# Performance work log

Hardware: AMD Instinct MI355X
Metric: run time of the kernel (lower is better)

Reference implementation:

```python
import jax, jax.numpy as jnp
import numpy as np

N, E, D = 50000, 800000, 128
H, C = 8, 16  # heads, hidden_per_head; H*C == D
NEG_SLOPE = 0.15


def setup_inputs() -> dict:
    key = jax.random.key(0)
    ks = jax.random.split(key, 8)
    x = jax.random.normal(ks[0], (N, D), dtype=jnp.float32)
    edge_index = jax.random.randint(ks[1], (2, E), 0, N, dtype=jnp.int32)
    s = 1.0 / np.sqrt(D)
    return {
        "x": x,
        "edge_index": edge_index,
        "ln_g": jnp.ones((D,), jnp.float32),
        "ln_b": jnp.zeros((D,), jnp.float32),
        "W_l": jax.random.normal(ks[2], (D, H * C), jnp.float32) * s,
        "b_l": jnp.zeros((H * C,), jnp.float32),
        "W_r": jax.random.normal(ks[3], (D, H * C), jnp.float32) * s,
        "b_r": jnp.zeros((H * C,), jnp.float32),
        "att": jax.random.normal(ks[4], (H, C), jnp.float32) * (1.0 / np.sqrt(C)),
        "bias": jnp.zeros((H * C,), jnp.float32),
    }


def _layernorm(x, g, b, eps=1e-5):
    mu = jnp.mean(x, axis=-1, keepdims=True)
    var = jnp.mean(jnp.square(x - mu), axis=-1, keepdims=True)
    return (x - mu) * jax.lax.rsqrt(var + eps) * g + b


def reference(x, edge_index, ln_g, ln_b, W_l, b_l, W_r, b_r, att, bias):
    src, dst = edge_index[0], edge_index[1]
    h = _layernorm(x, ln_g, ln_b)                      # [N, D]
    xl = (h @ W_l + b_l).reshape(N, H, C)              # source-side transform
    xr = (h @ W_r + b_r).reshape(N, H, C)              # target-side transform
    # GATv2 edge attention: leaky_relu(x_j + x_i) . att
    e = xl[src] + xr[dst]                              # [E, H, C]
    e_act = jnp.where(e > 0, e, NEG_SLOPE * e)
    alpha = jnp.einsum('ehc,hc->eh', e_act, att)       # [E, H]
    # segment softmax over edges grouped by destination node
    m = jax.ops.segment_max(alpha, dst, num_segments=N)   # [N, H]
    ex = jnp.exp(alpha - m[dst])                           # [E, H]
    denom = jax.ops.segment_sum(ex, dst, num_segments=N)  # [N, H]
    a = ex / (denom[dst] + 1e-16)                          # [E, H]
    # weighted message aggregation (scatter-add)
    msg = xl[src] * a[:, :, None]                          # [E, H, C]
    out = jax.ops.segment_sum(msg, dst, num_segments=N)   # [N, H, C]
    out = out.reshape(N, H * C) + bias
    h2 = jax.nn.relu(out)                                  # act='relu', dropout off (eval)
    return x + h2                                          # proj is Identity (in_dim == out_dim)
```

## Files before the change

### kernel.cpp

```cpp
#include <hip/hip_runtime.h>

typedef unsigned int uint32;
typedef __attribute__((ext_vector_type(4))) float f32x4;
typedef __attribute__((ext_vector_type(2))) float f32x2;
typedef __attribute__((ext_vector_type(8))) short bf16x8;

#define NEG_SLOPE 0.15f
#define GPB 1

__device__ __forceinline__ float2 bf2_to_f2(uint32 u) {
  union { uint32 i; float f; } a, b;
  a.i = u << 16;
  b.i = u & 0xffff0000u;
  return make_float2(a.f, b.f);
}

__device__ __forceinline__ f32x2 unpk(uint32 u) {
  union { uint32 i; float f; } lo, hi;
  lo.i = u << 16; hi.i = u & 0xffff0000u;
  f32x2 r; r.x = lo.f; r.y = hi.f; return r;
}

__device__ __forceinline__ f32x2 vmax2(f32x2 a, f32x2 b) {
  f32x2 r; r.x = fmaxf(a.x, b.x); r.y = fmaxf(a.y, b.y); return r;
}

__device__ __forceinline__ float bf_to_f(unsigned short s) {
  union { uint32 i; float f; } u;
  u.i = ((uint32)s) << 16;
  return u.f;
}

__device__ __forceinline__ unsigned short f32_to_bf16(float f) {
  union { float f; uint32 i; } u; u.f = f;
  uint32 r = u.i + 0x7fffu + ((u.i >> 16) & 1u);
  return (unsigned short)(r >> 16);
}

__device__ __forceinline__ uint32 pack_bf2(float x, float y) {
  return (uint32)f32_to_bf16(x) | ((uint32)f32_to_bf16(y) << 16);
}

__device__ __forceinline__ float2 loadpair(const void* p, size_t i, int isbf) {
  if (isbf) return bf2_to_f2(((const uint32*)p)[i]);
  return ((const float2*)p)[i];
}

__device__ __forceinline__ float loadelem(const void* p, size_t i, int isbf) {
  if (isbf) return bf_to_f(((const unsigned short*)p)[i]);
  return ((const float*)p)[i];
}

__device__ __forceinline__ int get_isbf(const void* ln_g) {
  return ((const uint32*)ln_g)[0] != 0x3F800000u ? 1 : 0;
}

__global__ __launch_bounds__(256) void prepAll_k(
    const void* __restrict__ Wl, const void* __restrict__ Wr,
    const void* __restrict__ bl, const void* __restrict__ br,
    const void* __restrict__ att, const void* __restrict__ obias,
    const void* __restrict__ ln_g, const void* __restrict__ ln_b,
    unsigned short* __restrict__ Wt, float* __restrict__ c1,
    float* __restrict__ c2b, float* __restrict__ att_c,
    float* __restrict__ obias_c)
{
  int isbf = get_isbf(ln_g);
  int b = blockIdx.x;
  if (b < 128) {
    int id = b * 256 + threadIdx.x;
    int n = id >> 7, k = id & 127;
    float g = loadelem(ln_g, k, isbf);
    float v = (n < 128) ? loadelem(Wl, (size_t)k * 128 + n, isbf)
                        : loadelem(Wr, (size_t)k * 128 + (n - 128), isbf);
    Wt[(size_t)n * 128 + k] = f32_to_bf16(g * v);
    if (id < 128) {
      att_c[id]   = loadelem(att, id, isbf);
      obias_c[id] = loadelem(obias, id, isbf);
    }
  } else {
    int w = threadIdx.x >> 6, lane = threadIdx.x & 63;
    int n = (b - 128) * 4 + w;
    const void* W = (n < 128) ? Wl : Wr;
    int nn = n & 127;
    float s1 = 0.f, s2 = 0.f;
    #pragma unroll
    for (int t = 0; t < 2; ++t) {
      int kk = t * 64 + lane;
      float wv = loadelem(W, (size_t)kk * 128 + nn, isbf);
      s1 += loadelem(ln_g, kk, isbf) * wv;
      s2 += loadelem(ln_b, kk, isbf) * wv;
    }
    #pragma unroll
    for (int off = 1; off < 64; off <<= 1) {
      s1 += __shfl_xor(s1, off, 64);
      s2 += __shfl_xor(s2, off, 64);
    }
    if (lane == 0) {
      c1[n] = s1;
      c2b[n] = s2 + ((n < 128) ? loadelem(bl, nn, isbf) : loadelem(br, nn, isbf));
    }
  }
}

__device__ __forceinline__ void load_group(bf16x8* slot, const void* x,
                                           int isbf, int rl, int quad) {
  if (isbf) {
    const unsigned short* xp = (const unsigned short*)x + (size_t)rl * 128 + quad * 8;
    #pragma unroll
    for (int kc = 0; kc < 4; ++kc) slot[kc] = *(const bf16x8*)(xp + kc * 32);
  } else {
    const float* xp = (const float*)x + (size_t)rl * 128 + quad * 8;
    #pragma unroll
    for (int kc = 0; kc < 4; ++kc) {
      float4 a0 = *(const float4*)(xp + kc * 32);
      float4 a1 = *(const float4*)(xp + kc * 32 + 4);
      union { bf16x8 v; uint32 u[4]; } av;
      av.u[0] = pack_bf2(a0.x, a0.y);
      av.u[1] = pack_bf2(a0.z, a0.w);
      av.u[2] = pack_bf2(a1.x, a1.y);
      av.u[3] = pack_bf2(a1.z, a1.w);
      slot[kc] = av.v;
    }
  }
}

__global__ __launch_bounds__(256) void ln_gemm_k(
    const void* __restrict__ x, const void* __restrict__ ln_g,
    const unsigned short* __restrict__ Wt,
    const float* __restrict__ c1, const float* __restrict__ c2b,
    unsigned short* __restrict__ xl,
    unsigned short* __restrict__ xr,
    int nrows)
{
  int isbf = get_isbf(ln_g);
  int lane = threadIdx.x & 63;
  int w    = threadIdx.x >> 6;
  int m16  = lane & 15;
  int quad = lane >> 4;
  int base = blockIdx.x * (GPB * 16);

  bf16x8 araw[GPB][4];
  #pragma unroll
  for (int g2 = 0; g2 < GPB; ++g2) {
    int r = base + g2 * 16 + m16;
    if (r >= nrows) r = nrows - 1;
    load_group(araw[g2], x, isbf, r, quad);
  }

  bf16x8 bfrag[4][4];
  #pragma unroll
  for (int nt = 0; nt < 4; ++nt)
    #pragma unroll
    for (int kc = 0; kc < 4; ++kc)
      bfrag[nt][kc] = *(const bf16x8*)(
          Wt + (size_t)(w * 64 + nt * 16 + m16) * 128 + kc * 32 + quad * 8);

  float c1v[4], c2v[4];
  #pragma unroll
  for (int nt = 0; nt < 4; ++nt) {
    int col = w * 64 + nt * 16 + m16;
    c1v[nt] = c1[col];
    c2v[nt] = c2b[col];
  }

  unsigned short* dst = (w < 2) ? xl : xr;
  int cb = (w & 1) * 64;

  #pragma unroll
  for (int g2 = 0; g2 < GPB; ++g2) {
    bf16x8* A = araw[g2];

    float s = 0.f, s2 = 0.f;
    #pragma unroll
    for (int kc = 0; kc < 4; ++kc) {
      union { bf16x8 v; uint32 u[4]; } uu; uu.v = A[kc];
      #pragma unroll
      for (int j = 0; j < 4; ++j) {
        float2 t = bf2_to_f2(uu.u[j]);
        s += t.x + t.y;
        s2 += t.x * t.x + t.y * t.y;
      }
    }
    s  += __shfl_xor(s, 16, 64);  s2 += __shfl_xor(s2, 16, 64);
    s  += __shfl_xor(s, 32, 64);  s2 += __shfl_xor(s2, 32, 64);
    float mu  = s * (1.0f / 128.0f);
    float var = fmaxf(s2 * (1.0f / 128.0f) - mu * mu, 0.0f);
    float rs  = rsqrtf(var + 1e-5f);
    float rm  = rs * mu;

    f32x4 acc[4];
    #pragma unroll
    for (int nt = 0; nt < 4; ++nt) acc[nt] = (f32x4){0.f, 0.f, 0.f, 0.f};
    #pragma unroll
    for (int kc = 0; kc < 4; ++kc)
      #pragma unroll
      for (int nt = 0; nt < 4; ++nt)
        acc[nt] = __builtin_amdgcn_mfma_f32_16x16x32_bf16(A[kc], bfrag[nt][kc], acc[nt], 0, 0, 0);

    float rs_j[4], rm_j[4];
    #pragma unroll
    for (int j = 0; j < 4; ++j) {
      rs_j[j] = __shfl(rs, quad * 4 + j, 64);
      rm_j[j] = __shfl(rm, quad * 4 + j, 64);
    }

    #pragma unroll
    for (int nt = 0; nt < 4; ++nt) {
      #pragma unroll
      for (int j = 0; j < 4; ++j) {
        int r = base + g2 * 16 + quad * 4 + j;
        if (r < nrows)
          dst[(size_t)r * 128 + cb + nt * 16 + m16] =
              f32_to_bf16(rs_j[j] * acc[nt][j] - rm_j[j] * c1v[nt] + c2v[nt]);
      }
    }
  }
}

__global__ __launch_bounds__(256) void hist_k(
    const int* __restrict__ ei, int* __restrict__ cntg,
    int E, int Eb, int R)
{
  __shared__ int hist[256];
  int b = blockIdx.x, tid = threadIdx.x;
  hist[tid] = 0;
  __syncthreads();
  int startE = b * Eb, endE = min(E, startE + Eb);
  const int* dp = ei + E;
  if (((E | startE) & 3) == 0) {
    int nfull = (endE - startE) >> 2;
    for (int g = tid; g < nfull; g += 256) {
      int4 d = *(const int4*)(dp + startE + g * 4);
      atomicAdd(&hist[((uint32)d.x) >> 8], 1);
      atomicAdd(&hist[((uint32)d.y) >> 8], 1);
      atomicAdd(&hist[((uint32)d.z) >> 8], 1);
      atomicAdd(&hist[((uint32)d.w) >> 8], 1);
    }
    int rem0 = startE + nfull * 4;
    if (rem0 + tid < endE) atomicAdd(&hist[((uint32)dp[rem0 + tid]) >> 8], 1);
  } else {
    for (int e = startE + tid; e < endE; e += 256)
      atomicAdd(&hist[((uint32)dp[e]) >> 8], 1);
  }
  __syncthreads();
  if (tid < R) cntg[tid * 256 + b] = hist[tid];
}

__global__ __launch_bounds__(1024) void scanA_k(const int* __restrict__ in,
    int* __restrict__ outl, int* __restrict__ psum, int n)
{
  __shared__ int wsum[16];
  int tid = threadIdx.x, lane = tid & 63, w = tid >> 6;
  int i = blockIdx.x * 1024 + tid;
  int v = (i < n) ? in[i] : 0;
  int xs = v;
  #pragma unroll
  for (int off = 1; off < 64; off <<= 1) {
    int y = __shfl_up(xs, off, 64);
    if (lane >= off) xs += y;
  }
  if (lane == 63) wsum[w] = xs;
  __syncthreads();
  if (w == 0) {
    int sv = (lane < 16) ? wsum[lane] : 0;
    int ss = sv;
    #pragma unroll
    for (int off = 1; off < 16; off <<= 1) {
      int y = __shfl_up(ss, off, 64);
      if (lane >= off) ss += y;
    }
    if (lane < 16) wsum[lane] = ss - sv;
    if (lane == 15) psum[blockIdx.x] = ss;
  }
  __syncthreads();
  if (i < n) outl[i] = wsum[w] + xs - v;
}

__global__ void scanB_k(int* __restrict__ psum, int* __restrict__ total, int nb) {
  int lane = threadIdx.x;
  int v = (lane < nb) ? psum[lane] : 0;
  int xs = v;
  #pragma unroll
  for (int off = 1; off < 64; off <<= 1) {
    int y = __shfl_up(xs, off, 64);
    if (lane >= off) xs += y;
  }
  if (lane < nb) psum[lane] = xs - v;
  if (lane == 63) *total = xs;
}

__global__ void scanC2_k(int* __restrict__ arr, const int* __restrict__ psum, int n) {
  int i = blockIdx.x * blockDim.x + threadIdx.x;
  if (i < n) arr[i] += psum[i >> 10];
}

__global__ __launch_bounds__(256) void binscatter_k(
    const int* __restrict__ ei, const int* __restrict__ cbase,
    uint32* __restrict__ binned, int E, int Eb, int R)
{
  __shared__ int cur[256];
  int b = blockIdx.x, tid = threadIdx.x;
  if (tid < R) cur[tid] = cbase[tid * 256 + b];
  __syncthreads();
  int startE = b * Eb, endE = min(E, startE + Eb);
  if (((E | startE) & 3) == 0) {
    int nfull = (endE - startE) >> 2;
    for (int g = tid; g < nfull; g += 256) {
      int e = startE + g * 4;
      int4 s = *(const int4*)(ei + e);
      int4 d = *(const int4*)(ei + E + e);
      int p0 = atomicAdd(&cur[((uint32)d.x) >> 8], 1);
      binned[p0] = (uint32)s.x | (((uint32)d.x & 255u) << 16);
      int p1 = atomicAdd(&cur[((uint32)d.y) >> 8], 1);
      binned[p1] = (uint32)s.y | (((uint32)d.y & 255u) << 16);
      int p2 = atomicAdd(&cur[((uint32)d.z) >> 8], 1);
      binned[p2] = (uint32)s.z | (((uint32)d.z & 255u) << 16);
      int p3 = atomicAdd(&cur[((uint32)d.w) >> 8], 1);
      binned[p3] = (uint32)s.w | (((uint32)d.w & 255u) << 16);
    }
    int rem0 = startE + nfull * 4;
    if (rem0 + tid < endE) {
      int e = rem0 + tid;
      uint32 src = (uint32)ei[e], dst = (uint32)ei[E + e];
      int pos = atomicAdd(&cur[dst >> 8], 1);
      binned[pos] = src | ((dst & 255u) << 16);
    }
  } else {
    for (int e = startE + tid; e < endE; e += 256) {
      uint32 src = (uint32)ei[e], dst = (uint32)ei[E + e];
      int pos = atomicAdd(&cur[dst >> 8], 1);
      binned[pos] = src | ((dst & 255u) << 16);
    }
  }
}

__global__ __launch_bounds__(256) void rangesort_k(
    const uint32* __restrict__ binned, const int* __restrict__ cbase,
    int* __restrict__ starts, unsigned short* __restrict__ csr16,
    int E, int N, int R)
{
  __shared__ int hist[256];
  __shared__ int wsum[4];
  __shared__ int cur[256];
  int r = blockIdx.x;
  int tid = threadIdx.x, lane = tid & 63, w = tid >> 6;
  int segStart = cbase[r * 256];
  int segEnd = (r + 1 < R) ? cbase[(r + 1) * 256] : E;

  hist[tid] = 0;
  __syncthreads();
  for (int i = segStart + tid; i < segEnd; i += 256)
    atomicAdd(&hist[(binned[i] >> 16) & 255u], 1);
  __syncthreads();

  int v = hist[tid];
  int xs = v;
  #pragma unroll
  for (int off = 1; off < 64; off <<= 1) {
    int y = __shfl_up(xs, off, 64);
    if (lane >= off) xs += y;
  }
  if (lane == 63) wsum[w] = xs;
  __syncthreads();
  int woff = 0;
  #pragma unroll
  for (int i = 0; i < 4; ++i) if (i < w) woff += wsum[i];
  int st = segStart + woff + xs - v;
  int node = (r << 8) + tid;
  if (node < N) starts[node] = st;
  cur[tid] = st;
  __syncthreads();

  for (int i = segStart + tid; i < segEnd; i += 256) {
    uint32 pk = binned[i];
    int d = (pk >> 16) & 255u;
    int pos = atomicAdd(&cur[d], 1);
    csr16[pos] = (unsigned short)(pk & 0xffffu);
  }
}

__global__ __launch_bounds__(256) void agg_k(
    const uint32* __restrict__ xl32,
    const uint32* __restrict__ xr32,
    const int* __restrict__ starts, const unsigned short* __restrict__ csr16,
    const void* __restrict__ x, const void* __restrict__ ln_g,
    const float* __restrict__ att_c, const float* __restrict__ obias_c,
    void* __restrict__ out, int n)
{
  int node = blockIdx.x * 4 + (threadIdx.x >> 6);
  if (node >= n) return;
  int isbf = get_isbf(ln_g);
  int lane = threadIdx.x & 63;
  int q    = lane >> 4;
  int sub  = lane & 15;

  uint4 xru = *(const uint4*)(xr32 + (size_t)node * 64 + sub * 4);
  f32x2 xr0 = unpk(xru.x), xr1 = unpk(xru.y), xr2 = unpk(xru.z), xr3 = unpk(xru.w);
  const f32x2* atp = (const f32x2*)(att_c + sub * 8);
  f32x2 t0 = atp[0], t1 = atp[1], t2 = atp[2], t3 = atp[3];
  f32x2 ns; ns.x = NEG_SLOPE; ns.y = NEG_SLOPE;

  float lsum = 0.f;
  f32x2 ac[4];
  #pragma unroll
  for (int i = 0; i < 4; ++i) { ac[i].x = 0.f; ac[i].y = 0.f; }

  int p0 = starts[node], p1 = starts[node + 1];
  if (p0 < p1) {
    int pmax = p1 - 1;
    int pe = p0 + q;
    bool valid = pe < p1;
    uint4 xu = *(const uint4*)(xl32 + (size_t)csr16[min(pe, pmax)] * 64 + sub * 4);

    for (int p = p0; p < p1; p += 4) {
      int pen = p + 4 + q;
      uint4 xun = *(const uint4*)(xl32 + (size_t)csr16[min(pen, pmax)] * 64 + sub * 4);

      f32x2 a0 = unpk(xu.x), a1 = unpk(xu.y), a2 = unpk(xu.z), a3 = unpk(xu.w);
      f32x2 e0 = a0 + xr0, e1 = a1 + xr1, e2 = a2 + xr2, e3 = a3 + xr3;
      e0 = vmax2(e0, e0 * ns);
      e1 = vmax2(e1, e1 * ns);
      e2 = vmax2(e2, e2 * ns);
      e3 = vmax2(e3, e3 * ns);
      f32x2 dt = e0 * t0;
      dt += e1 * t1;
      dt += e2 * t2;
      dt += e3 * t3;
      float dot = dt.x + dt.y;
      dot += __shfl_xor(dot, 1, 64);
      float pw = valid ? __expf(dot) : 0.f;
      lsum += pw;
      f32x2 pw2; pw2.x = pw; pw2.y = pw;
      ac[0] += pw2 * a0;
      ac[1] += pw2 * a1;
      ac[2] += pw2 * a2;
      ac[3] += pw2 * a3;

      xu = xun;
      valid = pen < p1;
    }
  }

  lsum += __shfl_xor(lsum, 16, 64);
  lsum += __shfl_xor(lsum, 32, 64);
  #pragma unroll
  for (int i = 0; i < 4; ++i) {
    ac[i].x += __shfl_xor(ac[i].x, 16, 64);
    ac[i].x += __shfl_xor(ac[i].x, 32, 64);
    ac[i].y += __shfl_xor(ac[i].y, 16, 64);
    ac[i].y += __shfl_xor(ac[i].y, 32, 64);
  }

  if (q == 0) {
    float inv = 1.0f / (lsum + 1e-16f);
    float4 b0 = *(const float4*)(obias_c + sub * 8);
    float4 b1 = *(const float4*)(obias_c + sub * 8 + 4);
    float2 rx[4];
    #pragma unroll
    for (int i = 0; i < 4; ++i)
      rx[i] = loadpair(x, (size_t)node * 64 + sub * 4 + i, isbf);
    float o0 = rx[0].x + fmaxf(ac[0].x * inv + b0.x, 0.f);
    float o1 = rx[0].y + fmaxf(ac[0].y * inv + b0.y, 0.f);
    float o2 = rx[1].x + fmaxf(ac[1].x * inv + b0.z, 0.f);
    float o3 = rx[1].y + fmaxf(ac[1].y * inv + b0.w, 0.f);
    float o4 = rx[2].x + fmaxf(ac[2].x * inv + b1.x, 0.f);
    float o5 = rx[2].y + fmaxf(ac[2].y * inv + b1.y, 0.f);
    float o6 = rx[3].x + fmaxf(ac[3].x * inv + b1.z, 0.f);
    float o7 = rx[3].y + fmaxf(ac[3].y * inv + b1.w, 0.f);
    if (isbf) {
      uint4 ov;
      ov.x = pack_bf2(o0, o1); ov.y = pack_bf2(o2, o3);
      ov.z = pack_bf2(o4, o5); ov.w = pack_bf2(o6, o7);
      *(uint4*)((uint32*)out + (size_t)node * 64 + sub * 4) = ov;
    } else {
      float4 f0 = make_float4(o0, o1, o2, o3);
      float4 f1 = make_float4(o4, o5, o6, o7);
      *(float4*)((float*)out + (size_t)node * 128 + sub * 8) = f0;
      *(float4*)((float*)out + (size_t)node * 128 + sub * 8 + 4) = f1;
    }
  }
}

static inline char* align16(char* p) {
  return (char*)(((uintptr_t)p + 15) & ~(uintptr_t)15);
}

extern "C" void kernel_launch(void* const* d_in, const int* in_sizes, int n_in,
                              void* d_out, int out_size, void* d_ws, size_t ws_size,
                              hipStream_t stream) {
  const void* x    = d_in[0];
  const int*  ei   = (const int*)d_in[1];
  const void* ln_g = d_in[2];
  const void* ln_b = d_in[3];
  const void* Wl   = d_in[4];
  const void* bl   = d_in[5];
  const void* Wr   = d_in[6];
  const void* br   = d_in[7];
  const void* att  = d_in[8];
  const void* bias = d_in[9];

  int N = in_sizes[0] / 128;
  int E = in_sizes[1] / 2;
  int R = (N + 255) >> 8;
  int L = R * 256;
  int Eb = (((E + 255) / 256) + 3) & ~3;

  char* ws = (char*)d_ws;
  unsigned short* xl = (unsigned short*)ws; ws = align16(ws + (size_t)N * 128 * 2);
  unsigned short* xr = (unsigned short*)ws; ws = align16(ws + (size_t)N * 128 * 2);
  unsigned short* Wt = (unsigned short*)ws; ws = align16(ws + 256 * 128 * 2);
  float* c1      = (float*)ws;              ws = align16(ws + 256 * 4);
  float* c2b     = (float*)ws;              ws = align16(ws + 256 * 4);
  float* att_c   = (float*)ws;              ws = align16(ws + 128 * 4);
  float* obias_c = (float*)ws;              ws = align16(ws + 128 * 4);
  int* cntg      = (int*)ws;                ws = align16(ws + (size_t)L * 4);
  int* cbase     = (int*)ws;                ws = align16(ws + (size_t)L * 4);
  int* psum      = (int*)ws;                ws = align16(ws + 64 * 4);
  int* starts    = (int*)ws;                ws = align16(ws + (size_t)(N + 1) * 4);
  uint32* binned = (uint32*)ws;             ws = align16(ws + (size_t)E * 4);
  unsigned short* csr16 = (unsigned short*)ws; ws = align16(ws + (size_t)E * 2);

  int nbScan = (L + 1023) / 1024;

  hipLaunchKernelGGL(prepAll_k, dim3(192), dim3(256), 0, stream,
                     Wl, Wr, bl, br, att, bias, ln_g, ln_b,
                     Wt, c1, c2b, att_c, obias_c);
  hipLaunchKernelGGL(hist_k, dim3(256), dim3(256), 0, stream, ei, cntg, E, Eb, R);
  hipLaunchKernelGGL(scanA_k, dim3(nbScan), dim3(1024), 0, stream, cntg, cbase, psum, L);
  hipLaunchKernelGGL(scanB_k, dim3(1), dim3(64), 0, stream, psum, starts + N, nbScan);
  hipLaunchKernelGGL(scanC2_k, dim3((L + 255) / 256), dim3(256), 0, stream, cbase, psum, L);
  hipLaunchKernelGGL(binscatter_k, dim3(256), dim3(256), 0, stream,
                     ei, cbase, binned, E, Eb, R);
  hipLaunchKernelGGL(rangesort_k, dim3(R), dim3(256), 0, stream,
                     binned, cbase, starts, csr16, E, N, R);
  hipLaunchKernelGGL(ln_gemm_k, dim3((N + GPB * 16 - 1) / (GPB * 16)), dim3(256), 0, stream,
                     x, ln_g, Wt, c1, c2b, xl, xr, N);
  hipLaunchKernelGGL(agg_k, dim3((N + 3) / 4), dim3(256), 0, stream,
                     (const uint32*)xl, (const uint32*)xr, starts, csr16,
                     x, ln_g, att_c, obias_c, d_out, N);
}
```

Measured before the change: 202.2 us.

## Fuse prep with histogram and binscatter with LN-GEMM, deepen agg prefetch

Merges the weight-prep kernel with the edge histogram into one launch, and the bin-scatter kernel with the layernorm+GEMM into one heterogeneous grid. The scan-add pass is removed by folding the block prefix into the consumers (binscatter and rangesort). GEMM blocks now process two row groups each, and the aggregation loop prefetches two edges ahead instead of one. This reduces launch count and serialization gaps and lets independent work overlap, at the cost of more register pressure. It also drops the unaligned fallback paths in the histogram and scatter kernels.

```diff
diff --git a/kernel.cpp b/kernel.cpp
--- a/kernel.cpp
+++ b/kernel.cpp
@@ -6,7 +6,7 @@
 typedef __attribute__((ext_vector_type(8))) short bf16x8;
 
 #define NEG_SLOPE 0.15f
-#define GPB 1
+#define GPB 2
 
 __device__ __forceinline__ float2 bf2_to_f2(uint32 u) {
   union { uint32 i; float f; } a, b;
@@ -55,18 +55,20 @@
   return ((const uint32*)ln_g)[0] != 0x3F800000u ? 1 : 0;
 }
 
-__global__ __launch_bounds__(256) void prepAll_k(
+__global__ __launch_bounds__(256) void prep_hist_k(
     const void* __restrict__ Wl, const void* __restrict__ Wr,
     const void* __restrict__ bl, const void* __restrict__ br,
     const void* __restrict__ att, const void* __restrict__ obias,
     const void* __restrict__ ln_g, const void* __restrict__ ln_b,
     unsigned short* __restrict__ Wt, float* __restrict__ c1,
     float* __restrict__ c2b, float* __restrict__ att_c,
-    float* __restrict__ obias_c)
+    float* __restrict__ obias_c,
+    const int* __restrict__ ei, int* __restrict__ cntg,
+    int E, int Eb, int R)
 {
-  int isbf = get_isbf(ln_g);
   int b = blockIdx.x;
   if (b < 128) {
+    int isbf = get_isbf(ln_g);
     int id = b * 256 + threadIdx.x;
     int n = id >> 7, k = id & 127;
     float g = loadelem(ln_g, k, isbf);
@@ -77,7 +79,8 @@
       att_c[id]   = loadelem(att, id, isbf);
       obias_c[id] = loadelem(obias, id, isbf);
     }
-  } else {
+  } else if (b < 192) {
+    int isbf = get_isbf(ln_g);
     int w = threadIdx.x >> 6, lane = threadIdx.x & 63;
     int n = (b - 128) * 4 + w;
     const void* W = (n < 128) ? Wl : Wr;
@@ -99,7 +102,69 @@
       c1[n] = s1;
       c2b[n] = s2 + ((n < 128) ? loadelem(bl, nn, isbf) : loadelem(br, nn, isbf));
     }
-  }
+  } else {
+    __shared__ int hist[256];
+    int hb = b - 192, tid = threadIdx.x;
+    hist[tid] = 0;
+    __syncthreads();
+    int startE = hb * Eb, endE = min(E, startE + Eb);
+    const int* dp = ei + E;
+    int nfull = (endE > startE) ? ((endE - startE) >> 2) : 0;
+    for (int g = tid; g < nfull; g += 256) {
+      int4 d = *(const int4*)(dp + startE + g * 4);
+      atomicAdd(&hist[((uint32)d.x) >> 8], 1);
+      atomicAdd(&hist[((uint32)d.y) >> 8], 1);
+      atomicAdd(&hist[((uint32)d.z) >> 8], 1);
+      atomicAdd(&hist[((uint32)d.w) >> 8], 1);
+    }
+    int rem0 = startE + nfull * 4;
+    if (rem0 + tid < endE) atomicAdd(&hist[((uint32)dp[rem0 + tid]) >> 8], 1);
+    __syncthreads();
+    if (tid < R) cntg[tid * 256 + hb] = hist[tid];
+  }
+}
+
+__global__ __launch_bounds__(1024) void scanA_k(const int* __restrict__ in,
+    int* __restrict__ outl, int* __restrict__ psum, int n)
+{
+  __shared__ int wsum[16];
+  int tid = threadIdx.x, lane = tid & 63, w = tid >> 6;
+  int i = blockIdx.x * 1024 + tid;
+  int v = (i < n) ? in[i] : 0;
+  int xs = v;
+  #pragma unroll
+  for (int off = 1; off < 64; off <<= 1) {
+    int y = __shfl_up(xs, off, 64);
+    if (lane >= off) xs += y;
+  }
+  if (lane == 63) wsum[w] = xs;
+  __syncthreads();
+  if (w == 0) {
+    int sv = (lane < 16) ? wsum[lane] : 0;
+    int ss = sv;
+    #pragma unroll
+    for (int off = 1; off < 16; off <<= 1) {
+      int y = __shfl_up(ss, off, 64);
+      if (lane >= off) ss += y;
+    }
+    if (lane < 16) wsum[lane] = ss - sv;
+    if (lane == 15) psum[blockIdx.x] = ss;
+  }
+  __syncthreads();
+  if (i < n) outl[i] = wsum[w] + xs - v;
+}
+
+__global__ void scanB_k(int* __restrict__ psum, int* __restrict__ total, int nb) {
+  int lane = threadIdx.x;
+  int v = (lane < nb) ? psum[lane] : 0;
+  int xs = v;
+  #pragma unroll
+  for (int off = 1; off < 64; off <<= 1) {
+    int y = __shfl_up(xs, off, 64);
+    if (lane >= off) xs += y;
+  }
+  if (lane < nb) psum[lane] = xs - v;
+  if (lane == 63) *total = xs;
 }
 
 __device__ __forceinline__ void load_group(bf16x8* slot, const void* x,
@@ -124,187 +189,26 @@
   }
 }
 
-__global__ __launch_bounds__(256) void ln_gemm_k(
+__global__ __launch_bounds__(256) void bin_gemm_k(
+    const int* __restrict__ ei, const int* __restrict__ cbase,
+    const int* __restrict__ psum, uint32* __restrict__ binned,
+    int E, int Eb, int R,
     const void* __restrict__ x, const void* __restrict__ ln_g,
     const unsigned short* __restrict__ Wt,
     const float* __restrict__ c1, const float* __restrict__ c2b,
-    unsigned short* __restrict__ xl,
-    unsigned short* __restrict__ xr,
+    unsigned short* __restrict__ xl, unsigned short* __restrict__ xr,
     int nrows)
 {
-  int isbf = get_isbf(ln_g);
-  int lane = threadIdx.x & 63;
-  int w    = threadIdx.x >> 6;
-  int m16  = lane & 15;
-  int quad = lane >> 4;
-  int base = blockIdx.x * (GPB * 16);
-
-  bf16x8 araw[GPB][4];
-  #pragma unroll
-  for (int g2 = 0; g2 < GPB; ++g2) {
-    int r = base + g2 * 16 + m16;
-    if (r >= nrows) r = nrows - 1;
-    load_group(araw[g2], x, isbf, r, quad);
-  }
-
-  bf16x8 bfrag[4][4];
-  #pragma unroll
-  for (int nt = 0; nt < 4; ++nt)
-    #pragma unroll
-    for (int kc = 0; kc < 4; ++kc)
-      bfrag[nt][kc] = *(const bf16x8*)(
-          Wt + (size_t)(w * 64 + nt * 16 + m16) * 128 + kc * 32 + quad * 8);
-
-  float c1v[4], c2v[4];
-  #pragma unroll
-  for (int nt = 0; nt < 4; ++nt) {
-    int col = w * 64 + nt * 16 + m16;
-    c1v[nt] = c1[col];
-    c2v[nt] = c2b[col];
-  }
-
-  unsigned short* dst = (w < 2) ? xl : xr;
-  int cb = (w & 1) * 64;
-
-  #pragma unroll
-  for (int g2 = 0; g2 < GPB; ++g2) {
-    bf16x8* A = araw[g2];
-
-    float s = 0.f, s2 = 0.f;
-    #pragma unroll
-    for (int kc = 0; kc < 4; ++kc) {
-      union { bf16x8 v; uint32 u[4]; } uu; uu.v = A[kc];
-      #pragma unroll
-      for (int j = 0; j < 4; ++j) {
-        float2 t = bf2_to_f2(uu.u[j]);
-        s += t.x + t.y;
-        s2 += t.x * t.x + t.y * t.y;
-      }
-    }
-    s  += __shfl_xor(s, 16, 64);  s2 += __shfl_xor(s2, 16, 64);
-    s  += __shfl_xor(s, 32, 64);  s2 += __shfl_xor(s2, 32, 64);
-    float mu  = s * (1.0f / 128.0f);
-    float var = fmaxf(s2 * (1.0f / 128.0f) - mu * mu, 0.0f);
-    float rs  = rsqrtf(var + 1e-5f);
-    float rm  = rs * mu;
-
-    f32x4 acc[4];
-    #pragma unroll
-    for (int nt = 0; nt < 4; ++nt) acc[nt] = (f32x4){0.f, 0.f, 0.f, 0.f};
-    #pragma unroll
-    for (int kc = 0; kc < 4; ++kc)
-      #pragma unroll
-      for (int nt = 0; nt < 4; ++nt)
-        acc[nt] = __builtin_amdgcn_mfma_f32_16x16x32_bf16(A[kc], bfrag[nt][kc], acc[nt], 0, 0, 0);
-
-    float rs_j[4], rm_j[4];
-    #pragma unroll
-    for (int j = 0; j < 4; ++j) {
-      rs_j[j] = __shfl(rs, quad * 4 + j, 64);
-      rm_j[j] = __shfl(rm, quad * 4 + j, 64);
-    }
-
-    #pragma unroll
-    for (int nt = 0; nt < 4; ++nt) {
-      #pragma unroll
-      for (int j = 0; j < 4; ++j) {
-        int r = base + g2 * 16 + quad * 4 + j;
-        if (r < nrows)
-          dst[(size_t)r * 128 + cb + nt * 16 + m16] =
-              f32_to_bf16(rs_j[j] * acc[nt][j] - rm_j[j] * c1v[nt] + c2v[nt]);
-      }
-    }
-  }
-}
-
-__global__ __launch_bounds__(256) void hist_k(
-    const int* __restrict__ ei, int* __restrict__ cntg,
-    int E, int Eb, int R)
-{
-  __shared__ int hist[256];
-  int b = blockIdx.x, tid = threadIdx.x;
-  hist[tid] = 0;
-  __syncthreads();
-  int startE = b * Eb, endE = min(E, startE + Eb);
-  const int* dp = ei + E;
-  if (((E | startE) & 3) == 0) {
-    int nfull = (endE - startE) >> 2;
-    for (int g = tid; g < nfull; g += 256) {
-      int4 d = *(const int4*)(dp + startE + g * 4);
-      atomicAdd(&hist[((uint32)d.x) >> 8], 1);
-      atomicAdd(&hist[((uint32)d.y) >> 8], 1);
-      atomicAdd(&hist[((uint32)d.z) >> 8], 1);
-      atomicAdd(&hist[((uint32)d.w) >> 8], 1);
-    }
-    int rem0 = startE + nfull * 4;
-    if (rem0 + tid < endE) atomicAdd(&hist[((uint32)dp[rem0 + tid]) >> 8], 1);
-  } else {
-    for (int e = startE + tid; e < endE; e += 256)
-      atomicAdd(&hist[((uint32)dp[e]) >> 8], 1);
-  }
-  __syncthreads();
-  if (tid < R) cntg[tid * 256 + b] = hist[tid];
-}
-
-__global__ __launch_bounds__(1024) void scanA_k(const int* __restrict__ in,
-    int* __restrict__ outl, int* __restrict__ psum, int n)
-{
-  __shared__ int wsum[16];
-  int tid = threadIdx.x, lane = tid & 63, w = tid >> 6;
-  int i = blockIdx.x * 1024 + tid;
-  int v = (i < n) ? in[i] : 0;
-  int xs = v;
-  #pragma unroll
-  for (int off = 1; off < 64; off <<= 1) {
-    int y = __shfl_up(xs, off, 64);
-    if (lane >= off) xs += y;
-  }
-  if (lane == 63) wsum[w] = xs;
-  __syncthreads();
-  if (w == 0) {
-    int sv = (lane < 16) ? wsum[lane] : 0;
-    int ss = sv;
-    #pragma unroll
-    for (int off = 1; off < 16; off <<= 1) {
-      int y = __shfl_up(ss, off, 64);
-      if (lane >= off) ss += y;
-    }
-    if (lane < 16) wsum[lane] = ss - sv;
-    if (lane == 15) psum[blockIdx.x] = ss;
-  }
-  __syncthreads();
-  if (i < n) outl[i] = wsum[w] + xs - v;
-}
-
-__global__ void scanB_k(int* __restrict__ psum, int* __restrict__ total, int nb) {
-  int lane = threadIdx.x;
-  int v = (lane < nb) ? psum[lane] : 0;
-  int xs = v;
-  #pragma unroll
-  for (int off = 1; off < 64; off <<= 1) {
-    int y = __shfl_up(xs, off, 64);
-    if (lane >= off) xs += y;
-  }
-  if (lane < nb) psum[lane] = xs - v;
-  if (lane == 63) *total = xs;
-}
-
-__global__ void scanC2_k(int* __restrict__ arr, const int* __restrict__ psum, int n) {
-  int i = blockIdx.x * blockDim.x + threadIdx.x;
-  if (i < n) arr[i] += psum[i >> 10];
-}
-
-__global__ __launch_bounds__(256) void binscatter_k(
-    const int* __restrict__ ei, const int* __restrict__ cbase,
-    uint32* __restrict__ binned, int E, int Eb, int R)
-{
-  __shared__ int cur[256];
-  int b = blockIdx.x, tid = threadIdx.x;
-  if (tid < R) cur[tid] = cbase[tid * 256 + b];
-  __syncthreads();
-  int startE = b * Eb, endE = min(E, startE + Eb);
-  if (((E | startE) & 3) == 0) {
-    int nfull = (endE - startE) >> 2;
+  if (blockIdx.x < 256) {
+    __shared__ int cur[256];
+    int b = blockIdx.x, tid = threadIdx.x;
+    if (tid < R) {
+      int idx = tid * 256 + b;
+      cur[tid] = cbase[idx] + psum[idx >> 10];
+    }
+    __syncthreads();
+    int startE = b * Eb, endE = min(E, startE + Eb);
+    int nfull = (endE > startE) ? ((endE - startE) >> 2) : 0;
     for (int g = tid; g < nfull; g += 256) {
       int e = startE + g * 4;
       int4 s = *(const int4*)(ei + e);
@@ -325,17 +229,98 @@
       int pos = atomicAdd(&cur[dst >> 8], 1);
       binned[pos] = src | ((dst & 255u) << 16);
     }
-  } else {
-    for (int e = startE + tid; e < endE; e += 256) {
-      uint32 src = (uint32)ei[e], dst = (uint32)ei[E + e];
-      int pos = atomicAdd(&cur[dst >> 8], 1);
-      binned[pos] = src | ((dst & 255u) << 16);
+    return;
+  }
+
+  int bid  = blockIdx.x - 256;
+  int isbf = get_isbf(ln_g);
+  int lane = threadIdx.x & 63;
+  int w    = threadIdx.x >> 6;
+  int m16  = lane & 15;
+  int quad = lane >> 4;
+  int base = bid * (GPB * 16);
+
+  bf16x8 araw[GPB][4];
+  #pragma unroll
+  for (int g2 = 0; g2 < GPB; ++g2) {
+    int r = base + g2 * 16 + m16;
+    if (r >= nrows) r = nrows - 1;
+    load_group(araw[g2], x, isbf, r, quad);
+  }
+
+  bf16x8 bfrag[4][4];
+  #pragma unroll
+  for (int nt = 0; nt < 4; ++nt)
+    #pragma unroll
+    for (int kc = 0; kc < 4; ++kc)
+      bfrag[nt][kc] = *(const bf16x8*)(
+          Wt + (size_t)(w * 64 + nt * 16 + m16) * 128 + kc * 32 + quad * 8);
+
+  float c1v[4], c2v[4];
+  #pragma unroll
+  for (int nt = 0; nt < 4; ++nt) {
+    int col = w * 64 + nt * 16 + m16;
+    c1v[nt] = c1[col];
+    c2v[nt] = c2b[col];
+  }
+
+  unsigned short* dst = (w < 2) ? xl : xr;
+  int cb = (w & 1) * 64;
+
+  #pragma unroll
+  for (int g2 = 0; g2 < GPB; ++g2) {
+    bf16x8* A = araw[g2];
+
+    float s = 0.f, s2 = 0.f;
+    #pragma unroll
+    for (int kc = 0; kc < 4; ++kc) {
+      union { bf16x8 v; uint32 u[4]; } uu; uu.v = A[kc];
+      #pragma unroll
+      for (int j = 0; j < 4; ++j) {
+        float2 t = bf2_to_f2(uu.u[j]);
+        s += t.x + t.y;
+        s2 += t.x * t.x + t.y * t.y;
+      }
+    }
+    s  += __shfl_xor(s, 16, 64);  s2 += __shfl_xor(s2, 16, 64);
+    s  += __shfl_xor(s, 32, 64);  s2 += __shfl_xor(s2, 32, 64);
+    float mu  = s * (1.0f / 128.0f);
+    float var = fmaxf(s2 * (1.0f / 128.0f) - mu * mu, 0.0f);
+    float rs  = rsqrtf(var + 1e-5f);
+    float rm  = rs * mu;
+
+    f32x4 acc[4];
+    #pragma unroll
+    for (int nt = 0; nt < 4; ++nt) acc[nt] = (f32x4){0.f, 0.f, 0.f, 0.f};
+    #pragma unroll
+    for (int kc = 0; kc < 4; ++kc)
+      #pragma unroll
+      for (int nt = 0; nt < 4; ++nt)
+        acc[nt] = __builtin_amdgcn_mfma_f32_16x16x32_bf16(A[kc], bfrag[nt][kc], acc[nt], 0, 0, 0);
+
+    float rs_j[4], rm_j[4];
+    #pragma unroll
+    for (int j = 0; j < 4; ++j) {
+      rs_j[j] = __shfl(rs, quad * 4 + j, 64);
+      rm_j[j] = __shfl(rm, quad * 4 + j, 64);
+    }
+
+    #pragma unroll
+    for (int nt = 0; nt < 4; ++nt) {
+      #pragma unroll
+      for (int j = 0; j < 4; ++j) {
+        int r = base + g2 * 16 + quad * 4 + j;
+        if (r < nrows)
+          dst[(size_t)r * 128 + cb + nt * 16 + m16] =
+              f32_to_bf16(rs_j[j] * acc[nt][j] - rm_j[j] * c1v[nt] + c2v[nt]);
+      }
     }
   }
 }
 
 __global__ __launch_bounds__(256) void rangesort_k(
     const uint32* __restrict__ binned, const int* __restrict__ cbase,
+    const int* __restrict__ psum,
     int* __restrict__ starts, unsigned short* __restrict__ csr16,
     int E, int N, int R)
 {
@@ -344,8 +329,15 @@
   __shared__ int cur[256];
   int r = blockIdx.x;
   int tid = threadIdx.x, lane = tid & 63, w = tid >> 6;
-  int segStart = cbase[r * 256];
-  int segEnd = (r + 1 < R) ? cbase[(r + 1) * 256] : E;
+  int i0 = r * 256;
+  int segStart = cbase[i0] + psum[i0 >> 10];
+  int segEnd;
+  if (r + 1 < R) {
+    int i1 = (r + 1) * 256;
+    segEnd = cbase[i1] + psum[i1 >> 10];
+  } else {
+    segEnd = E;
+  }
 
   hist[tid] = 0;
   __syncthreads();
@@ -408,13 +400,14 @@
   int p0 = starts[node], p1 = starts[node + 1];
   if (p0 < p1) {
     int pmax = p1 - 1;
-    int pe = p0 + q;
-    bool valid = pe < p1;
-    uint4 xu = *(const uint4*)(xl32 + (size_t)csr16[min(pe, pmax)] * 64 + sub * 4);
+    bool v0 = (p0 + q) < p1;
+    bool v1 = (p0 + 4 + q) < p1;
+    uint4 xu  = *(const uint4*)(xl32 + (size_t)csr16[min(p0 + q, pmax)] * 64 + sub * 4);
+    uint4 xu1 = *(const uint4*)(xl32 + (size_t)csr16[min(p0 + 4 + q, pmax)] * 64 + sub * 4);
 
     for (int p = p0; p < p1; p += 4) {
-      int pen = p + 4 + q;
-      uint4 xun = *(const uint4*)(xl32 + (size_t)csr16[min(pen, pmax)] * 64 + sub * 4);
+      int pe2 = p + 8 + q;
+      uint4 xu2 = *(const uint4*)(xl32 + (size_t)csr16[min(pe2, pmax)] * 64 + sub * 4);
 
       f32x2 a0 = unpk(xu.x), a1 = unpk(xu.y), a2 = unpk(xu.z), a3 = unpk(xu.w);
       f32x2 e0 = a0 + xr0, e1 = a1 + xr1, e2 = a2 + xr2, e3 = a3 + xr3;
@@ -428,7 +421,7 @@
       dt += e3 * t3;
       float dot = dt.x + dt.y;
       dot += __shfl_xor(dot, 1, 64);
-      float pw = valid ? __expf(dot) : 0.f;
+      float pw = v0 ? __expf(dot) : 0.f;
       lsum += pw;
       f32x2 pw2; pw2.x = pw; pw2.y = pw;
       ac[0] += pw2 * a0;
@@ -436,8 +429,8 @@
       ac[2] += pw2 * a2;
       ac[3] += pw2 * a3;
 
-      xu = xun;
-      valid = pen < p1;
+      xu = xu1; xu1 = xu2;
+      v0 = v1; v1 = pe2 < p1;
     }
   }
 
@@ -521,20 +514,19 @@
   unsigned short* csr16 = (unsigned short*)ws; ws = align16(ws + (size_t)E * 2);
 
   int nbScan = (L + 1023) / 1024;
-
-  hipLaunchKernelGGL(prepAll_k, dim3(192), dim3(256), 0, stream,
+  int nGemmB = (N + GPB * 16 - 1) / (GPB * 16);
+
+  hipLaunchKernelGGL(prep_hist_k, dim3(448), dim3(256), 0, stream,
                      Wl, Wr, bl, br, att, bias, ln_g, ln_b,
-                     Wt, c1, c2b, att_c, obias_c);
-  hipLaunchKernelGGL(hist_k, dim3(256), dim3(256), 0, stream, ei, cntg, E, Eb, R);
+                     Wt, c1, c2b, att_c, obias_c,
+                     ei, cntg, E, Eb, R);
   hipLaunchKernelGGL(scanA_k, dim3(nbScan), dim3(1024), 0, stream, cntg, cbase, psum, L);
   hipLaunchKernelGGL(scanB_k, dim3(1), dim3(64), 0, stream, psum, starts + N, nbScan);
-  hipLaunchKernelGGL(scanC2_k, dim3((L + 255) / 256), dim3(256), 0, stream, cbase, psum, L);
-  hipLaunchKernelGGL(binscatter_k, dim3(256), dim3(256), 0, stream,
-                     ei, cbase, binned, E, Eb, R);
+  hipLaunchKernelGGL(bin_gemm_k, dim3(256 + nGemmB), dim3(256), 0, stream,
+                     ei, cbase, psum, binned, E, Eb, R,
+                     x, ln_g, Wt, c1, c2b, xl, xr, N);
   hipLaunchKernelGGL(rangesort_k, dim3(R), dim3(256), 0, stream,
-                     binned, cbase, starts, csr16, E, N, R);
-  hipLaunchKernelGGL(ln_gemm_k, dim3((N + GPB * 16 - 1) / (GPB * 16)), dim3(256), 0, stream,
-                     x, ln_g, Wt, c1, c2b, xl, xr, N);
+                     binned, cbase, psum, starts, csr16, E, N, R);
   hipLaunchKernelGGL(agg_k, dim3((N + 3) / 4), dim3(256), 0, stream,
                      (const uint32*)xl, (const uint32*)xr, starts, csr16,
                      x, ln_g, att_c, obias_c, d_out, N);
```

New measurement: 182.8 us. -9.6%, faster.
